# Kernel optimization log

Hardware: AMD Instinct MI355X
Metric: run time of the kernel (lower is better)

## Reference

```python
import jax, jax.numpy as jnp
import numpy as np

K = 3
LAMBDA_AMP = 0.1
N_NODES = 100000
N_EDGES = 1600000
D_FEAT = 50


def _proximal_l21(x, lambda_):
    # rowwise L2,1 shrinkage: scale each row by max(||row||-lambda,0)/||row||
    row_norm = jnp.linalg.norm(x, axis=1)  # [N]
    score = jnp.maximum(row_norm - lambda_, 0.0)
    score = jnp.where(row_norm > 0, score / jnp.where(row_norm > 0, row_norm, 1.0), score)
    return score[:, None] * x


def setup_inputs() -> dict:
    key = jax.random.key(0)
    k1, k2, k3, k4 = jax.random.split(key, 4)
    feat = jax.random.normal(k1, (N_NODES, D_FEAT), dtype=jnp.float32)
    edge_weight = jax.random.uniform(k2, (N_EDGES,), dtype=jnp.float32)
    src = jax.random.randint(k3, (N_EDGES,), 0, N_NODES, dtype=jnp.int32)
    dst = jax.random.randint(k4, (N_EDGES,), 0, N_NODES, dtype=jnp.int32)
    return {"feat": feat, "edge_weight": edge_weight, "src": src, "dst": dst}


def reference(feat, edge_weight, src, dst):
    n = feat.shape[0]
    # add self-loops (add_self_loop=True), self-loop weight = 1
    loop = jnp.arange(n, dtype=src.dtype)
    src_f = jnp.concatenate([src, loop])
    dst_f = jnp.concatenate([dst, loop])
    ew = jnp.concatenate([edge_weight, jnp.ones((n,), dtype=edge_weight.dtype)])

    # norm='both': w_ji = ew / (sqrt(out_deg(j)) * sqrt(in_deg(i))), weighted degrees
    out_deg = jax.ops.segment_sum(ew, src_f, num_segments=n)
    in_deg = jax.ops.segment_sum(ew, dst_f, num_segments=n)
    inv_sqrt_out = jnp.where(out_deg > 0, out_deg, 1.0) ** -0.5 * (out_deg > 0)
    inv_sqrt_in = jnp.where(in_deg > 0, in_deg, 1.0) ** -0.5 * (in_deg > 0)
    w = ew * inv_sqrt_out[src_f] * inv_sqrt_in[dst_f]  # [E+N]

    lam = LAMBDA_AMP
    gamma = 1.0 / (2.0 * (1.0 - lam))
    hh = feat
    x = feat
    for _ in range(K):
        # compute_LX: x - A_norm x  (u_mul_e + sum == SpMM over edges)
        agg = jax.ops.segment_sum(x[src_f] * w[:, None], dst_f, num_segments=n)
        lx = x - agg
        y = x - gamma * 2.0 * (1.0 - lam) * lx
        x = hh + _proximal_l21(y - hh, gamma * lam)
    return x
```

## Files before the change

kernel.cpp:

```cpp
#include <hip/hip_runtime.h>
#include <hip/hip_bf16.h>
#include <hip/hip_fp16.h>

#define D 50
#define PADH 64
#define GLAM 0.05555555555555555f
#define SCAN_B 1024
#define FIXS 8388608.0f
#define INV_FIXS (1.0f / 8388608.0f)
#define WSC 32768.0f
#define INV_WSC (1.0f / 32768.0f)
#define EPB 8192
#define B2T 512
#define BSH 9
#define BMSK 511u
#define BT 512
#define MAXB 256
#define MAXRUN 12288

typedef unsigned long long u64;

__global__ void k_b1p(const int* __restrict__ src, const int* __restrict__ dst,
                      int* __restrict__ mat, const float* __restrict__ feat,
                      __half* __restrict__ xp, int e, int nblk, int nbuk, int n) {
    if ((int)blockIdx.x < nblk) {
        __shared__ unsigned hd[MAXB], hs[MAXB];
        for (int j = threadIdx.x; j < nbuk; j += blockDim.x) { hd[j] = 0; hs[j] = 0; }
        __syncthreads();
        int base = blockIdx.x * EPB;
        int end = base + EPB; if (end > e) end = e;
        for (int i = base + threadIdx.x; i < end; i += blockDim.x) {
            int t = __builtin_nontemporal_load(dst + i);
            int s = __builtin_nontemporal_load(src + i);
            atomicAdd(&hd[t >> BSH], 1u);
            atomicAdd(&hs[s >> BSH], 1u);
        }
        __syncthreads();
        for (int j = threadIdx.x; j < nbuk; j += blockDim.x) {
            mat[j * nblk + blockIdx.x] = (int)hd[j];
            mat[(nbuk + j) * nblk + blockIdx.x] = (int)hs[j];
        }
    } else {
        int i = ((int)blockIdx.x - nblk) * (int)blockDim.x + (int)threadIdx.x;
        if (i < n * PADH) {
            int node = i >> 6, col = i & 63;
            xp[i] = (col < D) ? __float2half_rn(feat[node * D + col]) : __half(0.0f);
        }
    }
}

__global__ void k_scan1(const int* __restrict__ cnt, int* __restrict__ out,
                        int* __restrict__ bsum, int n) {
    __shared__ int s[SCAN_B];
    int i = blockIdx.x * SCAN_B + threadIdx.x;
    int v = (i < n) ? cnt[i] : 0;
    s[threadIdx.x] = v; __syncthreads();
    for (int off = 1; off < SCAN_B; off <<= 1) {
        int t = (threadIdx.x >= (unsigned)off) ? s[threadIdx.x - off] : 0;
        __syncthreads();
        s[threadIdx.x] += t; __syncthreads();
    }
    if (i < n) out[i] = s[threadIdx.x] - v;
    if (threadIdx.x == SCAN_B - 1) bsum[blockIdx.x] = s[threadIdx.x];
}

__global__ void k_scan2(int* __restrict__ bsum, int nb) {
    __shared__ int s[SCAN_B];
    int v = (threadIdx.x < (unsigned)nb) ? bsum[threadIdx.x] : 0;
    s[threadIdx.x] = v; __syncthreads();
    for (int off = 1; off < SCAN_B; off <<= 1) {
        int t = (threadIdx.x >= (unsigned)off) ? s[threadIdx.x - off] : 0;
        __syncthreads();
        s[threadIdx.x] += t; __syncthreads();
    }
    if (threadIdx.x < (unsigned)nb) bsum[threadIdx.x] = s[threadIdx.x] - v;
}

__global__ void k_scan3(int* __restrict__ out, const int* __restrict__ bsum, int n) {
    int i = blockIdx.x * SCAN_B + threadIdx.x;
    if (i < n) out[i] += bsum[blockIdx.x];
}

__global__ void k_b2(const float* __restrict__ ew, const int* __restrict__ src,
                     const int* __restrict__ dst, const int* __restrict__ msc,
                     u64* __restrict__ bind, unsigned* __restrict__ bins,
                     int e, int nblk, int nbuk) {
    __shared__ unsigned cd[MAXB], cs[MAXB];
    __shared__ unsigned ld[MAXB], ls[MAXB];
    __shared__ int gbd[MAXB], gbs[MAXB];
    __shared__ u64 sd[EPB];
    __shared__ unsigned ss[EPB];
    __shared__ unsigned char bdd[EPB], bds[EPB];
    int tid = threadIdx.x;
    for (int j = tid; j < MAXB; j += blockDim.x) { cd[j] = 0; cs[j] = 0; }
    __syncthreads();
    int base = blockIdx.x * EPB;
    int end = base + EPB; if (end > e) end = e;
    int m = end - base;

    for (int i = base + tid; i < end; i += blockDim.x) {
        atomicAdd(&cd[(unsigned)__builtin_nontemporal_load(dst + i) >> BSH], 1u);
        atomicAdd(&cs[(unsigned)__builtin_nontemporal_load(src + i) >> BSH], 1u);
    }
    __syncthreads();

    unsigned vd = 0, vs = 0;
    if (tid < MAXB) { vd = cd[tid]; vs = cs[tid]; ld[tid] = vd; ls[tid] = vs; }
    __syncthreads();
    for (int off = 1; off < MAXB; off <<= 1) {
        unsigned td = 0, ts = 0;
        if (tid < MAXB && tid >= off) { td = ld[tid - off]; ts = ls[tid - off]; }
        __syncthreads();
        if (tid < MAXB) { ld[tid] += td; ls[tid] += ts; }
        __syncthreads();
    }
    if (tid < MAXB) {
        ld[tid] -= vd; ls[tid] -= vs;
        cd[tid] = ld[tid]; cs[tid] = ls[tid];
        if (tid < nbuk) {
            gbd[tid] = msc[tid * nblk + blockIdx.x];
            gbs[tid] = msc[(nbuk + tid) * nblk + blockIdx.x] - e;
        }
    }
    __syncthreads();

    for (int i = base + tid; i < end; i += blockDim.x) {
        float w = __builtin_nontemporal_load(ew + i);
        int s = __builtin_nontemporal_load(src + i);
        int t = __builtin_nontemporal_load(dst + i);
        unsigned wfix = (unsigned)(w * FIXS + 0.5f);
        if (wfix > 0x7FFFFFu) wfix = 0x7FFFFFu;
        unsigned tb = (unsigned)t >> BSH, sb = (unsigned)s >> BSH;
        unsigned pd = atomicAdd(&cd[tb], 1u);
        sd[pd] = ((u64)__float_as_uint(w) << 32)
               | ((unsigned)s << BSH) | (unsigned)(t & BMSK);
        bdd[pd] = (unsigned char)tb;
        unsigned ps = atomicAdd(&cs[sb], 1u);
        ss[ps] = (wfix << BSH) | (unsigned)(s & BMSK);
        bds[ps] = (unsigned char)sb;
    }
    __syncthreads();

    for (int p = tid; p < m; p += blockDim.x) {
        unsigned jd = bdd[p];
        bind[gbd[jd] + (int)(p - ld[jd])] = sd[p];
        unsigned js = bds[p];
        bins[gbs[js] + (int)(p - ls[js])] = ss[p];
    }
}

__global__ void k_srcdeg(const unsigned* __restrict__ bins, const int* __restrict__ msc,
                         float* __restrict__ iso, int n, int nblk, int nbuk, int e) {
    __shared__ unsigned wl[BT];
    wl[threadIdx.x] = 0;
    __syncthreads();
    int b = blockIdx.x;
    int start = msc[(nbuk + b) * nblk] - e;
    int end = (b + 1 < nbuk) ? (msc[(nbuk + b + 1) * nblk] - e) : e;
    for (int i = start + threadIdx.x; i < end; i += blockDim.x) {
        unsigned r = bins[i];
        atomicAdd(&wl[r & BMSK], r >> BSH);
    }
    __syncthreads();
    int node = b * BT + threadIdx.x;
    if (node < n)
        iso[node] = rsqrtf(1.0f + (float)wl[threadIdx.x] * INV_FIXS);
}

__global__ void k_dstfill(const u64* __restrict__ bind, const int* __restrict__ msc,
                          const float* __restrict__ iso, float* __restrict__ isi,
                          int* __restrict__ cnt, int* __restrict__ rowptr,
                          unsigned* __restrict__ pe, int n, int nblk, int nbuk, int e) {
    __shared__ u64 recs[MAXRUN];
    __shared__ unsigned cl[BT], wl[BT], cur[BT];
    __shared__ int sc[BT];
    __shared__ float isL[BT];
    cl[threadIdx.x] = 0; wl[threadIdx.x] = 0;
    __syncthreads();
    int b = blockIdx.x;
    int start = msc[b * nblk];
    int end = (b + 1 < nbuk) ? msc[(b + 1) * nblk] : e;
    int run = end - start;
    bool fast = (run <= MAXRUN);

    if (fast) {
        for (int i = threadIdx.x; i < run; i += blockDim.x) {
            u64 r = bind[start + i];
            recs[i] = r;
            unsigned loc = (unsigned)r & BMSK;
            float w = __uint_as_float((unsigned)(r >> 32));
            unsigned wfix = (unsigned)(w * FIXS + 0.5f);
            if (wfix > 0x7FFFFFu) wfix = 0x7FFFFFu;
            atomicAdd(&cl[loc], 1u);
            atomicAdd(&wl[loc], wfix);
        }
    } else {
        for (int i = start + threadIdx.x; i < end; i += blockDim.x) {
            u64 r = bind[i];
            unsigned loc = (unsigned)r & BMSK;
            float w = __uint_as_float((unsigned)(r >> 32));
            unsigned wfix = (unsigned)(w * FIXS + 0.5f);
            if (wfix > 0x7FFFFFu) wfix = 0x7FFFFFu;
            atomicAdd(&cl[loc], 1u);
            atomicAdd(&wl[loc], wfix);
        }
    }
    __syncthreads();

    int myc = (int)cl[threadIdx.x];
    sc[threadIdx.x] = myc;
    __syncthreads();
    for (int off = 1; off < BT; off <<= 1) {
        int t = (threadIdx.x >= (unsigned)off) ? sc[threadIdx.x - off] : 0;
        __syncthreads();
        sc[threadIdx.x] += t;
        __syncthreads();
    }
    int lrp = start + sc[threadIdx.x] - myc;

    float myisi = rsqrtf(1.0f + (float)wl[threadIdx.x] * INV_FIXS);
    isL[threadIdx.x] = myisi;
    cur[threadIdx.x] = (unsigned)lrp;

    int node = b * BT + threadIdx.x;
    if (node < n) {
        isi[node] = myisi;
        cnt[node] = myc;
        rowptr[node] = lrp;
    }
    __syncthreads();

    if (fast) {
        for (int i = threadIdx.x; i < run; i += blockDim.x) {
            u64 r = recs[i];
            unsigned lo = (unsigned)r;
            unsigned tloc = lo & BMSK;
            unsigned s = lo >> BSH;
            float w = __uint_as_float((unsigned)(r >> 32));
            float wv = w * iso[s] * isL[tloc];
            unsigned wq = (unsigned)(wv * WSC + 0.5f);
            if (wq > 32767u) wq = 32767u;
            unsigned pos = atomicAdd(&cur[tloc], 1u);
            pe[pos] = (s << 15) | wq;
        }
    } else {
        for (int i = start + threadIdx.x; i < end; i += blockDim.x) {
            u64 r = bind[i];
            unsigned lo = (unsigned)r;
            unsigned tloc = lo & BMSK;
            unsigned s = lo >> BSH;
            float w = __uint_as_float((unsigned)(r >> 32));
            float wv = w * iso[s] * isL[tloc];
            unsigned wq = (unsigned)(wv * WSC + 0.5f);
            if (wq > 32767u) wq = 32767u;
            unsigned pos = atomicAdd(&cur[tloc], 1u);
            pe[pos] = (s << 15) | wq;
        }
    }
}

__device__ __forceinline__ void acc_edge(const uint4& u, float w,
                                         float& a0, float& a1, float& a2, float& a3,
                                         float& a4, float& a5, float& a6, float& a7) {
    const __half2* hp = (const __half2*)&u;
    float2 f0 = __half22float2(hp[0]);
    float2 f1 = __half22float2(hp[1]);
    float2 f2 = __half22float2(hp[2]);
    float2 f3 = __half22float2(hp[3]);
    a0 = fmaf(w, f0.x, a0); a1 = fmaf(w, f0.y, a1);
    a2 = fmaf(w, f1.x, a2); a3 = fmaf(w, f1.y, a3);
    a4 = fmaf(w, f2.x, a4); a5 = fmaf(w, f2.y, a5);
    a6 = fmaf(w, f3.x, a6); a7 = fmaf(w, f3.y, a7);
}

__global__ void k_iter(const int* __restrict__ rowptr, const int* __restrict__ cnt,
                       const unsigned* __restrict__ pe, const __half* __restrict__ xin,
                       const __half* __restrict__ xpF, const float* __restrict__ iso,
                       const float* __restrict__ isi, __half* __restrict__ hout,
                       float* __restrict__ fout, int n, int final_iter) {
    int lane = threadIdx.x & 63;
    int c    = lane & 7;
    int waveId = (blockIdx.x * blockDim.x + threadIdx.x) >> 6;
    int node = waveId * 8 + (lane >> 3);
    if (node >= n) return;

    float a0 = 0.f, a1 = 0.f, a2 = 0.f, a3 = 0.f;
    float a4 = 0.f, a5 = 0.f, a6 = 0.f, a7 = 0.f;

    int beg = rowptr[node], m = cnt[node];

    int j = 0;
    for (; j + 4 <= m; j += 4) {
        unsigned p0 = pe[beg + j];
        unsigned p1 = pe[beg + j + 1];
        unsigned p2 = pe[beg + j + 2];
        unsigned p3 = pe[beg + j + 3];
        unsigned s0 = p0 >> 15; float w0 = (float)(p0 & 32767u) * INV_WSC;
        unsigned s1 = p1 >> 15; float w1 = (float)(p1 & 32767u) * INV_WSC;
        unsigned s2 = p2 >> 15; float w2 = (float)(p2 & 32767u) * INV_WSC;
        unsigned s3 = p3 >> 15; float w3 = (float)(p3 & 32767u) * INV_WSC;
        uint4 u0 = *(const uint4*)(xin + ((size_t)s0 << 6) + (c << 3));
        uint4 u1 = *(const uint4*)(xin + ((size_t)s1 << 6) + (c << 3));
        uint4 u2 = *(const uint4*)(xin + ((size_t)s2 << 6) + (c << 3));
        uint4 u3 = *(const uint4*)(xin + ((size_t)s3 << 6) + (c << 3));
        acc_edge(u0, w0, a0, a1, a2, a3, a4, a5, a6, a7);
        acc_edge(u1, w1, a0, a1, a2, a3, a4, a5, a6, a7);
        acc_edge(u2, w2, a0, a1, a2, a3, a4, a5, a6, a7);
        acc_edge(u3, w3, a0, a1, a2, a3, a4, a5, a6, a7);
    }
    for (; j < m; ++j) {
        unsigned p0 = pe[beg + j];
        unsigned s0 = p0 >> 15;
        float    w0 = (float)(p0 & 32767u) * INV_WSC;
        uint4 u0 = *(const uint4*)(xin + ((size_t)s0 << 6) + (c << 3));
        acc_edge(u0, w0, a0, a1, a2, a3, a4, a5, a6, a7);
    }

    float selfw = iso[node] * isi[node];
    {
        uint4 u = *(const uint4*)(xin + ((size_t)node << 6) + (c << 3));
        acc_edge(u, selfw, a0, a1, a2, a3, a4, a5, a6, a7);
    }

    float f[8];
    {
        uint4 u = *(const uint4*)(xpF + ((size_t)node << 6) + (c << 3));
        const __half2* hp = (const __half2*)&u;
        float2 f0 = __half22float2(hp[0]);
        float2 f1 = __half22float2(hp[1]);
        float2 f2 = __half22float2(hp[2]);
        float2 f3 = __half22float2(hp[3]);
        f[0] = f0.x; f[1] = f0.y; f[2] = f1.x; f[3] = f1.y;
        f[4] = f2.x; f[5] = f2.y; f[6] = f3.x; f[7] = f3.y;
    }

    float d0 = a0 - f[0], d1 = a1 - f[1], d2 = a2 - f[2], d3 = a3 - f[3];
    float d4 = a4 - f[4], d5 = a5 - f[5], d6 = a6 - f[6], d7 = a7 - f[7];

    float ssum = d0*d0 + d1*d1 + d2*d2 + d3*d3 + d4*d4 + d5*d5 + d6*d6 + d7*d7;
    ssum += __shfl_xor(ssum, 1, 64);
    ssum += __shfl_xor(ssum, 2, 64);
    ssum += __shfl_xor(ssum, 4, 64);
    float norm = sqrtf(ssum);
    float sc = (norm > 0.0f) ? fmaxf(norm - GLAM, 0.0f) / norm : 0.0f;

    float o0 = f[0] + sc * d0, o1 = f[1] + sc * d1;
    float o2 = f[2] + sc * d2, o3 = f[3] + sc * d3;
    float o4 = f[4] + sc * d4, o5 = f[5] + sc * d5;
    float o6 = f[6] + sc * d6, o7 = f[7] + sc * d7;
    if (!final_iter) {
        __half2 h0 = __float22half2_rn(make_float2(o0, o1));
        __half2 h1 = __float22half2_rn(make_float2(o2, o3));
        __half2 h2 = __float22half2_rn(make_float2(o4, o5));
        __half2 h3 = __float22half2_rn(make_float2(o6, o7));
        uint4 u;
        u.x = *(unsigned*)&h0; u.y = *(unsigned*)&h1;
        u.z = *(unsigned*)&h2; u.w = *(unsigned*)&h3;
        *(uint4*)(hout + ((size_t)node << 6) + (c << 3)) = u;
    } else {
        float o[8] = {o0, o1, o2, o3, o4, o5, o6, o7};
        int fb = c << 3;
        #pragma unroll
        for (int k = 0; k < 4; ++k) {
            int ff = fb + (k << 1);
            if (ff + 1 < D) {
                float2 v; v.x = o[k * 2]; v.y = o[k * 2 + 1];
                *(float2*)(fout + (size_t)node * D + ff) = v;
            }
        }
    }
}

extern "C" void kernel_launch(void* const* d_in, const int* in_sizes, int n_in,
                              void* d_out, int out_size, void* d_ws, size_t ws_size,
                              hipStream_t stream) {
    const float* feat = (const float*)d_in[0];
    const float* ew   = (const float*)d_in[1];
    const int* src = (const int*)d_in[2];
    const int* dst = (const int*)d_in[3];

    const int nd = in_sizes[0];
    const int n  = nd / D;
    const int e  = in_sizes[1];
    const int np = n * PADH;

    const int nbuk = (n + BT - 1) / BT;
    const int nblk = (e + EPB - 1) / EPB;
    const int nm   = 2 * nbuk * nblk;

    __half*   xpF    = (__half*)d_ws;
    __half*   xpA    = xpF + np;
    __half*   xpB    = xpA + np;
    u64*      bind   = (u64*)(xpB + np);
    unsigned* pe     = (unsigned*)(bind + e);
    unsigned* bins   = pe + e;
    int*      mat    = (int*)(bins + e);
    int*      msc    = mat + nm;
    float*    isi    = (float*)(msc + nm);
    float*    iso    = isi + n;
    int*      cnt    = (int*)(iso + n);
    int*      rowptr = cnt + n;
    int*      bsum   = rowptr + n;
    float*    out    = (float*)d_out;

    const int B = 256;
    const int gP  = (np + B2T - 1) / B2T;
    const int NBm = (nm + SCAN_B - 1) / SCAN_B;

    k_b1p<<<nblk + gP, B2T, 0, stream>>>(src, dst, mat, feat, xpF, e, nblk, nbuk, n);
    k_scan1<<<NBm, SCAN_B, 0, stream>>>(mat, msc, bsum, nm);
    k_scan2<<<1, SCAN_B, 0, stream>>>(bsum, NBm);
    k_scan3<<<NBm, SCAN_B, 0, stream>>>(msc, bsum, nm);
    k_b2<<<nblk, B2T, 0, stream>>>(ew, src, dst, msc, bind, bins, e, nblk, nbuk);
    k_srcdeg<<<nbuk, BT, 0, stream>>>(bins, msc, iso, n, nblk, nbuk, e);
    k_dstfill<<<nbuk, BT, 0, stream>>>(bind, msc, iso, isi, cnt, rowptr, pe, n, nblk, nbuk, e);

    const int nodesPerBlock = (B / 64) * 8;
    const int iterGrid = (n + nodesPerBlock - 1) / nodesPerBlock;

    k_iter<<<iterGrid, B, 0, stream>>>(rowptr, cnt, pe, xpF, xpF, iso, isi, xpA, out, n, 0);
    k_iter<<<iterGrid, B, 0, stream>>>(rowptr, cnt, pe, xpA, xpF, iso, isi, xpB, out, n, 0);
    k_iter<<<iterGrid, B, 0, stream>>>(rowptr, cnt, pe, xpB, xpF, iso, isi, xpA, out, n, 1);
}
```

Measured before the change: 254.5 us.

## Halve bucket chunk size, swizzle blocks across XCDs, stage CSR writes in LDS, unroll SpMM

Halves the edges per block in the bucketing pass and remaps block indices so consecutive chunks land on the same XCD, with launch bounds added to k_b2. In the dst-fill kernel the edge records are no longer cached in LDS. The packed CSR entries are scattered into an LDS staging buffer and then written to global memory contiguously, which replaces scattered global stores. The SpMM gather loop gains an 8-way unrolled section to keep more loads in flight, at the cost of re-reading bind from global and higher register use.

```diff
diff --git a/kernel.cpp b/kernel.cpp
--- a/kernel.cpp
+++ b/kernel.cpp
@@ -10,13 +10,14 @@
 #define INV_FIXS (1.0f / 8388608.0f)
 #define WSC 32768.0f
 #define INV_WSC (1.0f / 32768.0f)
-#define EPB 8192
+#define EPB 4096
 #define B2T 512
 #define BSH 9
 #define BMSK 511u
 #define BT 512
 #define MAXB 256
 #define MAXRUN 12288
+#define NXCD 8
 
 typedef unsigned long long u64;
 
@@ -81,7 +82,14 @@
     if (i < n) out[i] += bsum[blockIdx.x];
 }
 
-__global__ void k_b2(const float* __restrict__ ew, const int* __restrict__ src,
+__device__ __forceinline__ int xcd_swz(int p, int nwg) {
+    int q = nwg / NXCD, r = nwg % NXCD;
+    int xcd = p % NXCD, idx = p / NXCD;
+    return (xcd < r ? xcd * (q + 1) : r * (q + 1) + (xcd - r) * q) + idx;
+}
+
+__global__ __launch_bounds__(B2T, 4) void k_b2(
+                     const float* __restrict__ ew, const int* __restrict__ src,
                      const int* __restrict__ dst, const int* __restrict__ msc,
                      u64* __restrict__ bind, unsigned* __restrict__ bins,
                      int e, int nblk, int nbuk) {
@@ -92,9 +100,10 @@
     __shared__ unsigned ss[EPB];
     __shared__ unsigned char bdd[EPB], bds[EPB];
     int tid = threadIdx.x;
+    int wb = xcd_swz((int)blockIdx.x, nblk);
     for (int j = tid; j < MAXB; j += blockDim.x) { cd[j] = 0; cs[j] = 0; }
     __syncthreads();
-    int base = blockIdx.x * EPB;
+    int base = wb * EPB;
     int end = base + EPB; if (end > e) end = e;
     int m = end - base;
 
@@ -118,8 +127,8 @@
         ld[tid] -= vd; ls[tid] -= vs;
         cd[tid] = ld[tid]; cs[tid] = ls[tid];
         if (tid < nbuk) {
-            gbd[tid] = msc[tid * nblk + blockIdx.x];
-            gbs[tid] = msc[(nbuk + tid) * nblk + blockIdx.x] - e;
+            gbd[tid] = msc[tid * nblk + wb];
+            gbs[tid] = msc[(nbuk + tid) * nblk + wb] - e;
         }
     }
     __syncthreads();
@@ -171,7 +180,7 @@
                           const float* __restrict__ iso, float* __restrict__ isi,
                           int* __restrict__ cnt, int* __restrict__ rowptr,
                           unsigned* __restrict__ pe, int n, int nblk, int nbuk, int e) {
-    __shared__ u64 recs[MAXRUN];
+    __shared__ unsigned pst[MAXRUN];
     __shared__ unsigned cl[BT], wl[BT], cur[BT];
     __shared__ int sc[BT];
     __shared__ float isL[BT];
@@ -183,27 +192,14 @@
     int run = end - start;
     bool fast = (run <= MAXRUN);
 
-    if (fast) {
-        for (int i = threadIdx.x; i < run; i += blockDim.x) {
-            u64 r = bind[start + i];
-            recs[i] = r;
-            unsigned loc = (unsigned)r & BMSK;
-            float w = __uint_as_float((unsigned)(r >> 32));
-            unsigned wfix = (unsigned)(w * FIXS + 0.5f);
-            if (wfix > 0x7FFFFFu) wfix = 0x7FFFFFu;
-            atomicAdd(&cl[loc], 1u);
-            atomicAdd(&wl[loc], wfix);
-        }
-    } else {
-        for (int i = start + threadIdx.x; i < end; i += blockDim.x) {
-            u64 r = bind[i];
-            unsigned loc = (unsigned)r & BMSK;
-            float w = __uint_as_float((unsigned)(r >> 32));
-            unsigned wfix = (unsigned)(w * FIXS + 0.5f);
-            if (wfix > 0x7FFFFFu) wfix = 0x7FFFFFu;
-            atomicAdd(&cl[loc], 1u);
-            atomicAdd(&wl[loc], wfix);
-        }
+    for (int i = start + threadIdx.x; i < end; i += blockDim.x) {
+        u64 r = bind[i];
+        unsigned loc = (unsigned)r & BMSK;
+        float w = __uint_as_float((unsigned)(r >> 32));
+        unsigned wfix = (unsigned)(w * FIXS + 0.5f);
+        if (wfix > 0x7FFFFFu) wfix = 0x7FFFFFu;
+        atomicAdd(&cl[loc], 1u);
+        atomicAdd(&wl[loc], wfix);
     }
     __syncthreads();
 
@@ -216,11 +212,12 @@
         sc[threadIdx.x] += t;
         __syncthreads();
     }
-    int lrp = start + sc[threadIdx.x] - myc;
+    int lex = sc[threadIdx.x] - myc;
+    int lrp = start + lex;
 
     float myisi = rsqrtf(1.0f + (float)wl[threadIdx.x] * INV_FIXS);
     isL[threadIdx.x] = myisi;
-    cur[threadIdx.x] = (unsigned)lrp;
+    cur[threadIdx.x] = fast ? (unsigned)lex : (unsigned)lrp;
 
     int node = b * BT + threadIdx.x;
     if (node < n) {
@@ -231,8 +228,8 @@
     __syncthreads();
 
     if (fast) {
-        for (int i = threadIdx.x; i < run; i += blockDim.x) {
-            u64 r = recs[i];
+        for (int i = start + threadIdx.x; i < end; i += blockDim.x) {
+            u64 r = bind[i];
             unsigned lo = (unsigned)r;
             unsigned tloc = lo & BMSK;
             unsigned s = lo >> BSH;
@@ -241,8 +238,11 @@
             unsigned wq = (unsigned)(wv * WSC + 0.5f);
             if (wq > 32767u) wq = 32767u;
             unsigned pos = atomicAdd(&cur[tloc], 1u);
-            pe[pos] = (s << 15) | wq;
-        }
+            pst[pos] = (s << 15) | wq;
+        }
+        __syncthreads();
+        for (int p = threadIdx.x; p < run; p += blockDim.x)
+            pe[start + p] = pst[p];
     } else {
         for (int i = start + threadIdx.x; i < end; i += blockDim.x) {
             u64 r = bind[i];
@@ -290,6 +290,40 @@
     int beg = rowptr[node], m = cnt[node];
 
     int j = 0;
+    for (; j + 8 <= m; j += 8) {
+        unsigned p0 = pe[beg + j];
+        unsigned p1 = pe[beg + j + 1];
+        unsigned p2 = pe[beg + j + 2];
+        unsigned p3 = pe[beg + j + 3];
+        unsigned p4 = pe[beg + j + 4];
+        unsigned p5 = pe[beg + j + 5];
+        unsigned p6 = pe[beg + j + 6];
+        unsigned p7 = pe[beg + j + 7];
+        unsigned s0 = p0 >> 15; float w0 = (float)(p0 & 32767u) * INV_WSC;
+        unsigned s1 = p1 >> 15; float w1 = (float)(p1 & 32767u) * INV_WSC;
+        unsigned s2 = p2 >> 15; float w2 = (float)(p2 & 32767u) * INV_WSC;
+        unsigned s3 = p3 >> 15; float w3 = (float)(p3 & 32767u) * INV_WSC;
+        unsigned s4 = p4 >> 15; float w4 = (float)(p4 & 32767u) * INV_WSC;
+        unsigned s5 = p5 >> 15; float w5 = (float)(p5 & 32767u) * INV_WSC;
+        unsigned s6 = p6 >> 15; float w6 = (float)(p6 & 32767u) * INV_WSC;
+        unsigned s7 = p7 >> 15; float w7 = (float)(p7 & 32767u) * INV_WSC;
+        uint4 u0 = *(const uint4*)(xin + ((size_t)s0 << 6) + (c << 3));
+        uint4 u1 = *(const uint4*)(xin + ((size_t)s1 << 6) + (c << 3));
+        uint4 u2 = *(const uint4*)(xin + ((size_t)s2 << 6) + (c << 3));
+        uint4 u3 = *(const uint4*)(xin + ((size_t)s3 << 6) + (c << 3));
+        uint4 u4 = *(const uint4*)(xin + ((size_t)s4 << 6) + (c << 3));
+        uint4 u5 = *(const uint4*)(xin + ((size_t)s5 << 6) + (c << 3));
+        uint4 u6 = *(const uint4*)(xin + ((size_t)s6 << 6) + (c << 3));
+        uint4 u7 = *(const uint4*)(xin + ((size_t)s7 << 6) + (c << 3));
+        acc_edge(u0, w0, a0, a1, a2, a3, a4, a5, a6, a7);
+        acc_edge(u1, w1, a0, a1, a2, a3, a4, a5, a6, a7);
+        acc_edge(u2, w2, a0, a1, a2, a3, a4, a5, a6, a7);
+        acc_edge(u3, w3, a0, a1, a2, a3, a4, a5, a6, a7);
+        acc_edge(u4, w4, a0, a1, a2, a3, a4, a5, a6, a7);
+        acc_edge(u5, w5, a0, a1, a2, a3, a4, a5, a6, a7);
+        acc_edge(u6, w6, a0, a1, a2, a3, a4, a5, a6, a7);
+        acc_edge(u7, w7, a0, a1, a2, a3, a4, a5, a6, a7);
+    }
     for (; j + 4 <= m; j += 4) {
         unsigned p0 = pe[beg + j];
         unsigned p1 = pe[beg + j + 1];
```

Result: faster. 240.9 us (-5.4%).
